# Kernel optimization log

Measured on AMD Instinct MI355X. Metric: run time of the kernel, lower is better.

## Reference

```python
import jax, jax.numpy as jnp
import numpy as np
from jax import lax

N_VOX = 100000   # occupied voxels
GRID = 160       # dense grid extent per axis
K = 5            # kernel size -> 125 offsets
K3 = K * K * K
IMG_C, PTS_C, OUT_C = 64, 32, 16
EPS = 1e-5


def _build_coords_and_kernel_map():
    """Random unique voxel coords + kernel map: nbr[n,k] = row index of voxel at
    coords[n]+offset[k], or N_VOX (sentinel -> zero feature) if unoccupied."""
    rng = np.random.default_rng(0)
    flat = rng.choice(GRID ** 3, size=N_VOX, replace=False)
    coords = np.stack(np.unravel_index(flat, (GRID, GRID, GRID)), axis=1).astype(np.int64)
    B = GRID + 4  # shift coords by +2 so offsets in [-2,2] never wrap
    enc = ((coords[:, 0] + 2) * B + (coords[:, 1] + 2)) * B + (coords[:, 2] + 2)
    order = np.argsort(enc)
    enc_s = enc[order]
    offs = np.stack(np.meshgrid(np.arange(-2, 3), np.arange(-2, 3), np.arange(-2, 3), indexing='ij'), axis=-1).reshape(-1, 3)
    nbr = np.full((N_VOX, K3), N_VOX, dtype=np.int32)
    for k, (dx, dy, dz) in enumerate(offs):
        qe = enc + ((dx * B + dy) * B + dz)
        pos = np.clip(np.searchsorted(enc_s, qe), 0, N_VOX - 1)
        hit = enc_s[pos] == qe
        nbr[:, k] = np.where(hit, order[pos].astype(np.int32), np.int32(N_VOX))
    return nbr


def setup_inputs() -> dict:
    nbr_idx = jnp.asarray(_build_coords_and_kernel_map())
    key = jax.random.key(0)
    ks = jax.random.split(key, 20)
    def w(k, shape, fan):
        return jax.random.normal(k, shape, jnp.float32) * (1.0 / np.sqrt(fan))
    def bn(k0, k1, k2, k3):
        g = jax.random.uniform(k0, (OUT_C,), jnp.float32) + 0.5
        b = jax.random.normal(k1, (OUT_C,), jnp.float32) * 0.1
        m = jax.random.normal(k2, (OUT_C,), jnp.float32) * 0.1
        v = jax.random.uniform(k3, (OUT_C,), jnp.float32) + 0.5
        return g, b, m, v
    bn_img = bn(ks[2], ks[3], ks[4], ks[5])
    bn_pts = bn(ks[7], ks[8], ks[9], ks[10])
    bn_vis = bn(ks[12], ks[13], ks[14], ks[15])
    return {
        'img_voxel_feats': jax.random.normal(ks[0], (N_VOX, IMG_C), jnp.float32),
        'pts_voxel_feats': jax.random.normal(ks[1], (N_VOX, PTS_C), jnp.float32),
        'nbr_idx': nbr_idx,
        'W_img': w(ks[16], (K3, IMG_C, OUT_C), K3 * IMG_C),
        'bn_img_g': bn_img[0], 'bn_img_b': bn_img[1], 'bn_img_m': bn_img[2], 'bn_img_v': bn_img[3],
        'W_pts': w(ks[17], (K3, PTS_C, OUT_C), K3 * PTS_C),
        'bn_pts_g': bn_pts[0], 'bn_pts_b': bn_pts[1], 'bn_pts_m': bn_pts[2], 'bn_pts_v': bn_pts[3],
        'W_vis1': w(ks[18], (K3, 2 * OUT_C, OUT_C), K3 * 2 * OUT_C),
        'bn_vis_g': bn_vis[0], 'bn_vis_b': bn_vis[1], 'bn_vis_m': bn_vis[2], 'bn_vis_v': bn_vis[3],
        'W_vis2': w(ks[19], (OUT_C, 1), OUT_C),
    }


def _sparse_conv(feats, W, nbr_idx):
    # gather-GEMM-scatter sparse conv; sentinel row N -> zero feature
    feats_pad = jnp.concatenate([feats, jnp.zeros((1, feats.shape[1]), feats.dtype)], axis=0)
    init = jnp.zeros((feats.shape[0], W.shape[2]), feats.dtype)
    def step(acc, wk_ik):
        W_k, idx_k = wk_ik  # [Cin,Cout], [N]
        return acc + feats_pad[idx_k] @ W_k, None
    out, _ = lax.scan(step, init, (W, nbr_idx.T))
    return out


def _bn_relu(x, g, b, m, v):
    return jax.nn.relu((x - m) * (g * lax.rsqrt(v + EPS)) + b)


def reference(img_voxel_feats, pts_voxel_feats, nbr_idx,
              W_img, bn_img_g, bn_img_b, bn_img_m, bn_img_v,
              W_pts, bn_pts_g, bn_pts_b, bn_pts_m, bn_pts_v,
              W_vis1, bn_vis_g, bn_vis_b, bn_vis_m, bn_vis_v,
              W_vis2):
    img = _bn_relu(_sparse_conv(img_voxel_feats, W_img, nbr_idx), bn_img_g, bn_img_b, bn_img_m, bn_img_v)
    pts = _bn_relu(_sparse_conv(pts_voxel_feats, W_pts, nbr_idx), bn_pts_g, bn_pts_b, bn_pts_m, bn_pts_v)
    cat = jnp.concatenate([img, pts], axis=1)  # [N, 2*OUT_C]
    h = _bn_relu(_sparse_conv(cat, W_vis1, nbr_idx), bn_vis_g, bn_vis_b, bn_vis_m, bn_vis_v)
    vis_w = jax.nn.sigmoid(h @ W_vis2)  # [N,1]
    return vis_w * img + (1.0 - vis_w) * pts
```

## Files before the change

kernel.cpp:

```cpp
#include <hip/hip_runtime.h>

#define N_VOX 100000
#define K3 125
#define CENTER_K 62
#define BVOX 128
#define NBLK 782
#define EPSF 1e-5f

#define WIT 0
#define WPT 128000
#define WVT 192000
#define LST 256000
#define CAT (256000 + NBLK * 1024)

#define DOT4(f_, g_) ((f_).x*(g_).x + (f_).y*(g_).y + (f_).z*(g_).z + (f_).w*(g_).w)

__global__ __launch_bounds__(256) void prep_transpose(
    const float* __restrict__ Wi, const float* __restrict__ Wp,
    const float* __restrict__ Wv, float* __restrict__ ws)
{
    int i = blockIdx.x * 256 + threadIdx.x;
    if (i < 125 * 64 * 16) {
        int k = i >> 10, r = i & 1023;
        int c = r >> 4, o = r & 15;
        int cs = c >> 4, t = (c >> 2) & 3, e = c & 3;
        ws[WIT + k * 1024 + t * 256 + (cs * 16 + o) * 4 + e] = Wi[i];
    }
    if (i < 125 * 32 * 16) {
        int k = i / 512, r = i % 512;
        int c = r >> 4, o = r & 15;
        int cs = c >> 3, t = (c >> 2) & 1, e = c & 3;
        ws[WPT + k * 512 + t * 256 + (cs * 16 + o) * 4 + e] = Wp[i];
        ws[WVT + k * 512 + t * 256 + (cs * 16 + o) * 4 + e] = Wv[i];
    }
}

__global__ __launch_bounds__(512, 6) void convA(
    const float* __restrict__ fimg, const float* __restrict__ fpts,
    const int* __restrict__ nbr, float* __restrict__ ws,
    const float* __restrict__ gi, const float* __restrict__ bi,
    const float* __restrict__ mi, const float* __restrict__ vi,
    const float* __restrict__ gp, const float* __restrict__ bp,
    const float* __restrict__ mp, const float* __restrict__ vp)
{
    __shared__ int s_kcnt[128];
    __shared__ int s_scan[128];
    __shared__ int s_koff[128];
    __shared__ int s_list[768];
    __shared__ float s_acc[BVOX][32];
    __shared__ int s_next;

    const int tid = threadIdx.x, lane = tid & 63, wv = tid >> 6;
    const int blk = blockIdx.x;
    const int gbase = blk * BVOX;
    const int vcount = min(BVOX, N_VOX - gbase);
    const int q = lane >> 4;

    if (tid < 128) s_kcnt[tid] = 0;
    if (tid == 0) s_next = 0;
    __syncthreads();

    const int TOTE = vcount * K3;
    const int* nrow = nbr + (size_t)gbase * K3;
    for (int e = tid; e < TOTE; e += 512) {
        int idx = nrow[e];
        int k = e % K3;
        if (idx < N_VOX && k != CENTER_K) atomicAdd(&s_kcnt[k], 1);
    }
    __syncthreads();

    if (tid < 128) s_scan[tid] = (tid < K3) ? s_kcnt[tid] : 0;
    __syncthreads();
    for (int d = 1; d < 128; d <<= 1) {
        int v = 0;
        if (tid < 128 && tid >= d) v = s_scan[tid - d];
        __syncthreads();
        if (tid < 128) s_scan[tid] += v;
        __syncthreads();
    }
    if (tid < 128) s_koff[tid] = (tid == 0) ? 0 : s_scan[tid - 1];
    __syncthreads();
    if (tid < 128) s_kcnt[tid] = s_koff[tid];
    __syncthreads();

    for (int e = tid; e < TOTE; e += 512) {
        int idx = nrow[e];
        int k = e % K3;
        if (idx < N_VOX && k != CENTER_K) {
            int ln = e / K3;
            int pos = atomicAdd(&s_kcnt[k], 1);
            s_list[pos] = (ln << 17) | idx;
        }
    }
    __syncthreads();

    {
        int tot = s_koff[K3];
        int* dst = (int*)(ws + LST) + (size_t)blk * 1024;
        if (tid < 126) dst[tid] = s_koff[tid];
        for (int p = tid; p < tot; p += 512) dst[128 + p] = s_list[p];
    }

    const float4* __restrict__ fi4 = (const float4*)fimg;
    const float4* __restrict__ fp4 = (const float4*)fpts;

    {
        float4 cwi[4], cwp[2];
        const float4* WI4 = (const float4*)(ws + WIT + CENTER_K * 1024);
        const float4* WP4 = (const float4*)(ws + WPT + CENTER_K * 512);
        #pragma unroll
        for (int t = 0; t < 4; ++t) cwi[t] = WI4[t * 64 + lane];
        #pragma unroll
        for (int t = 0; t < 2; ++t) cwp[t] = WP4[t * 64 + lane];
        for (int i = 0; i < 16; ++i) {
            int ln = wv * 16 + i;
            if (ln >= vcount) break;
            int n = gbase + ln;
            const float4* fr = fi4 + (size_t)n * 16 + q * 4;
            const float4* gr = fp4 + (size_t)n * 8 + q * 2;
            float aI = DOT4(fr[0], cwi[0]) + DOT4(fr[1], cwi[1])
                     + DOT4(fr[2], cwi[2]) + DOT4(fr[3], cwi[3]);
            float aP = DOT4(gr[0], cwp[0]) + DOT4(gr[1], cwp[1]);
            aI += __shfl_xor(aI, 16); aI += __shfl_xor(aI, 32);
            aP += __shfl_xor(aP, 16); aP += __shfl_xor(aP, 32);
            if (lane < 32) s_acc[ln][lane] = (lane < 16) ? aI : aP;
        }
    }
    __syncthreads();

    while (true) {
        int s;
        if (lane == 0) s = atomicAdd(&s_next, 1);
        s = __shfl(s, 0);
        if (s >= K3) break;
        int pbeg = s_koff[s], pend = s_koff[s + 1];
        if (pbeg == pend) continue;
        float4 swi[4], swp[2];
        const float4* WI4 = (const float4*)(ws + WIT + s * 1024);
        const float4* WP4 = (const float4*)(ws + WPT + s * 512);
        #pragma unroll
        for (int t = 0; t < 4; ++t) swi[t] = WI4[t * 64 + lane];
        #pragma unroll
        for (int t = 0; t < 2; ++t) swp[t] = WP4[t * 64 + lane];
        for (int p = pbeg; p < pend; ++p) {
            int ent = s_list[p];
            int ln = ent >> 17, j = ent & 0x1FFFF;
            const float4* fr = fi4 + (size_t)j * 16 + q * 4;
            const float4* gr = fp4 + (size_t)j * 8 + q * 2;
            float aI = DOT4(fr[0], swi[0]) + DOT4(fr[1], swi[1])
                     + DOT4(fr[2], swi[2]) + DOT4(fr[3], swi[3]);
            float aP = DOT4(gr[0], swp[0]) + DOT4(gr[1], swp[1]);
            aI += __shfl_xor(aI, 16); aI += __shfl_xor(aI, 32);
            aP += __shfl_xor(aP, 16); aP += __shfl_xor(aP, 32);
            if (lane < 32) atomicAdd(&s_acc[ln][lane], (lane < 16) ? aI : aP);
        }
    }
    __syncthreads();

    {
        int c = tid & 31;
        float g, b, m, v;
        if (c < 16) { g = gi[c]; b = bi[c]; m = mi[c]; v = vi[c]; }
        else        { g = gp[c - 16]; b = bp[c - 16]; m = mp[c - 16]; v = vp[c - 16]; }
        float sc = g * rsqrtf(v + EPSF);
        float* cat = ws + CAT;
        for (int r = 0; r < 8; ++r) {
            int ln = (tid >> 5) + r * 16;
            if (ln < vcount)
                cat[(size_t)(gbase + ln) * 32 + c] =
                    fmaxf((s_acc[ln][c] - m) * sc + b, 0.f);
        }
    }
}

__global__ __launch_bounds__(512, 6) void convB(
    float* __restrict__ ws,
    const float* __restrict__ gv, const float* __restrict__ bv,
    const float* __restrict__ mv, const float* __restrict__ vv,
    const float* __restrict__ w2, float* __restrict__ out)
{
    __shared__ int s_koff[128];
    __shared__ int s_list[768];
    __shared__ float s_acc[BVOX][16];
    __shared__ int s_next;

    const int tid = threadIdx.x, lane = tid & 63, wv = tid >> 6;
    const int blk = blockIdx.x;
    const int gbase = blk * BVOX;
    const int vcount = min(BVOX, N_VOX - gbase);
    const int q = lane >> 4, o = lane & 15;

    const int* src = (const int*)(ws + LST) + (size_t)blk * 1024;
    if (tid < 126) s_koff[tid] = src[tid];
    if (tid == 0) s_next = 0;
    __syncthreads();
    int tot = s_koff[K3];
    for (int p = tid; p < tot; p += 512) s_list[p] = src[128 + p];

    const float4* __restrict__ c4 = (const float4*)(ws + CAT);

    {
        float4 cwv[2];
        const float4* WV4 = (const float4*)(ws + WVT + CENTER_K * 512);
        #pragma unroll
        for (int t = 0; t < 2; ++t) cwv[t] = WV4[t * 64 + lane];
        for (int i = 0; i < 16; ++i) {
            int ln = wv * 16 + i;
            if (ln >= vcount) break;
            int n = gbase + ln;
            const float4* cr = c4 + (size_t)n * 8 + q * 2;
            float aV = DOT4(cr[0], cwv[0]) + DOT4(cr[1], cwv[1]);
            aV += __shfl_xor(aV, 16); aV += __shfl_xor(aV, 32);
            if (lane < 16) s_acc[ln][o] = aV;
        }
    }
    __syncthreads();

    while (true) {
        int s;
        if (lane == 0) s = atomicAdd(&s_next, 1);
        s = __shfl(s, 0);
        if (s >= K3) break;
        int pbeg = s_koff[s], pend = s_koff[s + 1];
        if (pbeg == pend) continue;
        float4 swv[2];
        const float4* WV4 = (const float4*)(ws + WVT + s * 512);
        #pragma unroll
        for (int t = 0; t < 2; ++t) swv[t] = WV4[t * 64 + lane];
        for (int p = pbeg; p < pend; ++p) {
            int ent = s_list[p];
            int ln = ent >> 17, j = ent & 0x1FFFF;
            const float4* cr = c4 + (size_t)j * 8 + q * 2;
            float aV = DOT4(cr[0], swv[0]) + DOT4(cr[1], swv[1]);
            aV += __shfl_xor(aV, 16); aV += __shfl_xor(aV, 32);
            if (lane < 16) atomicAdd(&s_acc[ln][o], aV);
        }
    }
    __syncthreads();

    {
        float sV = gv[o] * rsqrtf(vv[o] + EPSF);
        float bV = bv[o], mV = mv[o], w2_ = w2[o];
        const float* cat = ws + CAT;
        for (int r = 0; r < 4; ++r) {
            int ln = (tid >> 4) + r * 32;
            float h = 0.f, xi = 0.f, xp = 0.f;
            if (ln < vcount) {
                int n = gbase + ln;
                h = fmaxf((s_acc[ln][o] - mV) * sV + bV, 0.f);
                xi = cat[(size_t)n * 32 + o];
                xp = cat[(size_t)n * 32 + 16 + o];
            }
            float ph = h * w2_;
            ph += __shfl_xor(ph, 1); ph += __shfl_xor(ph, 2);
            ph += __shfl_xor(ph, 4); ph += __shfl_xor(ph, 8);
            if (ln < vcount) {
                float vis = 1.f / (1.f + expf(-ph));
                out[(size_t)(gbase + ln) * 16 + o] = vis * xi + (1.f - vis) * xp;
            }
        }
    }
}

extern "C" void kernel_launch(void* const* d_in, const int* in_sizes, int n_in,
                              void* d_out, int out_size, void* d_ws, size_t ws_size,
                              hipStream_t stream) {
    const float* fimg = (const float*)d_in[0];
    const float* fpts = (const float*)d_in[1];
    const int*   nbr  = (const int*)d_in[2];
    const float* Wimg = (const float*)d_in[3];
    const float* gi = (const float*)d_in[4];
    const float* bi = (const float*)d_in[5];
    const float* mi = (const float*)d_in[6];
    const float* vi = (const float*)d_in[7];
    const float* Wpts = (const float*)d_in[8];
    const float* gp = (const float*)d_in[9];
    const float* bp = (const float*)d_in[10];
    const float* mp = (const float*)d_in[11];
    const float* vp = (const float*)d_in[12];
    const float* Wvis = (const float*)d_in[13];
    const float* gv = (const float*)d_in[14];
    const float* bv = (const float*)d_in[15];
    const float* mv = (const float*)d_in[16];
    const float* vv = (const float*)d_in[17];
    const float* w2 = (const float*)d_in[18];
    float* out = (float*)d_out;
    float* ws = (float*)d_ws;

    hipLaunchKernelGGL(prep_transpose, dim3(500), dim3(256), 0, stream,
                       Wimg, Wpts, Wvis, ws);
    hipLaunchKernelGGL(convA, dim3(NBLK), dim3(512), 0, stream,
                       fimg, fpts, nbr, ws, gi, bi, mi, vi, gp, bp, mp, vp);
    hipLaunchKernelGGL(convB, dim3(NBLK), dim3(512), 0, stream,
                       ws, gv, bv, mv, vv, w2, out);
}
```

Measured before the change: 229.7 us.

## Build per-block neighbor lists in separate compacting kernel, halve block size

Moves the kernel-map scan out of convA into a separate global build kernel that compacts valid (k, local voxel, neighbor) entries per block with global atomics, so convA only reads the short compacted list instead of rescanning 125 entries per voxel twice. Also changes the weight layout so each half-wave handles one gather (two pairs processed per wave with 32 lanes each), and shrinks blocks to 256 threads. The list is capped at 640 entries per block, so any overflow would silently drop neighbors, and an extra memset plus kernel launch is added.

```diff
diff --git a/kernel.cpp b/kernel.cpp
--- a/kernel.cpp
+++ b/kernel.cpp
@@ -3,15 +3,19 @@
 #define N_VOX 100000
 #define K3 125
 #define CENTER_K 62
-#define BVOX 128
+#define TVOX 128
 #define NBLK 782
+#define CAP2 640
 #define EPSF 1e-5f
 
 #define WIT 0
 #define WPT 128000
 #define WVT 192000
-#define LST 256000
-#define CAT (256000 + NBLK * 1024)
+#define GCNT 256000
+#define GLIST 257024
+#define KOFF  757504
+#define SLIST 857600
+#define CAT   1358080
 
 #define DOT4(f_, g_) ((f_).x*(g_).x + (f_).y*(g_).y + (f_).z*(g_).z + (f_).w*(g_).w)
 
@@ -22,150 +26,177 @@
     int i = blockIdx.x * 256 + threadIdx.x;
     if (i < 125 * 64 * 16) {
         int k = i >> 10, r = i & 1023;
-        int c = r >> 4, o = r & 15;
-        int cs = c >> 4, t = (c >> 2) & 3, e = c & 3;
-        ws[WIT + k * 1024 + t * 256 + (cs * 16 + o) * 4 + e] = Wi[i];
+        int c = r >> 4, oo = r & 15;
+        int qq = c >> 5, t = (c >> 2) & 7, e = c & 3;
+        ws[WIT + k * 1024 + t * 128 + (qq * 16 + oo) * 4 + e] = Wi[i];
     }
     if (i < 125 * 32 * 16) {
-        int k = i / 512, r = i % 512;
-        int c = r >> 4, o = r & 15;
-        int cs = c >> 3, t = (c >> 2) & 1, e = c & 3;
-        ws[WPT + k * 512 + t * 256 + (cs * 16 + o) * 4 + e] = Wp[i];
-        ws[WVT + k * 512 + t * 256 + (cs * 16 + o) * 4 + e] = Wv[i];
-    }
-}
-
-__global__ __launch_bounds__(512, 6) void convA(
+        int k = i >> 9, r = i & 511;
+        int c = r >> 4, oo = r & 15;
+        int qq = c >> 4, t = (c >> 2) & 3, e = c & 3;
+        ws[WPT + k * 512 + t * 128 + (qq * 16 + oo) * 4 + e] = Wp[i];
+        ws[WVT + k * 512 + t * 128 + (qq * 16 + oo) * 4 + e] = Wv[i];
+    }
+}
+
+__global__ __launch_bounds__(256) void build(const int* __restrict__ nbr,
+                                             float* __restrict__ ws)
+{
+    int* gcnt = (int*)(ws + GCNT);
+    int* glist = (int*)(ws + GLIST);
+    const int TOT4 = (N_VOX * K3) / 4;
+    const int4* n4 = (const int4*)nbr;
+    for (int i4 = blockIdx.x * 256 + threadIdx.x; i4 < TOT4; i4 += gridDim.x * 256) {
+        int4 v = n4[i4];
+        int base = i4 * 4;
+        int idxs[4] = {v.x, v.y, v.z, v.w};
+        #pragma unroll
+        for (int j = 0; j < 4; ++j) {
+            int idx = idxs[j];
+            int i = base + j;
+            unsigned n = (unsigned)i / K3;
+            int k = i - (int)n * K3;
+            if (idx < N_VOX && k != CENTER_K) {
+                int blk = n >> 7, ln = n & 127;
+                int pos = atomicAdd(&gcnt[blk], 1);
+                if (pos < CAP2)
+                    glist[(size_t)blk * CAP2 + pos] = (k << 24) | (ln << 17) | idx;
+            }
+        }
+    }
+}
+
+__global__ __launch_bounds__(256, 3) void convA(
     const float* __restrict__ fimg, const float* __restrict__ fpts,
-    const int* __restrict__ nbr, float* __restrict__ ws,
+    float* __restrict__ ws,
     const float* __restrict__ gi, const float* __restrict__ bi,
     const float* __restrict__ mi, const float* __restrict__ vi,
     const float* __restrict__ gp, const float* __restrict__ bp,
     const float* __restrict__ mp, const float* __restrict__ vp)
 {
     __shared__ int s_kcnt[128];
-    __shared__ int s_scan[128];
     __shared__ int s_koff[128];
-    __shared__ int s_list[768];
-    __shared__ float s_acc[BVOX][32];
+    __shared__ int s_list[CAP2];
+    __shared__ float s_acc[TVOX][32];
     __shared__ int s_next;
 
-    const int tid = threadIdx.x, lane = tid & 63, wv = tid >> 6;
-    const int blk = blockIdx.x;
-    const int gbase = blk * BVOX;
-    const int vcount = min(BVOX, N_VOX - gbase);
-    const int q = lane >> 4;
+    const int tid = threadIdx.x;
+    const int lane = tid & 63, wv = tid >> 6;
+    const int l32 = lane & 31, qp = (lane >> 4) & 1, o = lane & 15, s2 = lane >> 5;
+    const int blk = blockIdx.x, gbase = blk * TVOX;
+    const int vcount = min(TVOX, N_VOX - gbase);
 
     if (tid < 128) s_kcnt[tid] = 0;
     if (tid == 0) s_next = 0;
     __syncthreads();
 
-    const int TOTE = vcount * K3;
-    const int* nrow = nbr + (size_t)gbase * K3;
-    for (int e = tid; e < TOTE; e += 512) {
-        int idx = nrow[e];
-        int k = e % K3;
-        if (idx < N_VOX && k != CENTER_K) atomicAdd(&s_kcnt[k], 1);
-    }
-    __syncthreads();
-
-    if (tid < 128) s_scan[tid] = (tid < K3) ? s_kcnt[tid] : 0;
+    const int cnt = min(((const int*)(ws + GCNT))[blk], CAP2);
+    const int* gl = (const int*)(ws + GLIST) + (size_t)blk * CAP2;
+
+    for (int p = tid; p < cnt; p += 256)
+        atomicAdd(&s_kcnt[((unsigned)gl[p]) >> 24], 1);
+    __syncthreads();
+
+    if (tid < 128) s_koff[tid] = (tid < K3) ? s_kcnt[tid] : 0;
     __syncthreads();
     for (int d = 1; d < 128; d <<= 1) {
         int v = 0;
-        if (tid < 128 && tid >= d) v = s_scan[tid - d];
+        if (tid < 128 && tid >= d) v = s_koff[tid - d];
         __syncthreads();
-        if (tid < 128) s_scan[tid] += v;
+        if (tid < 128) s_koff[tid] += v;
         __syncthreads();
     }
-    if (tid < 128) s_koff[tid] = (tid == 0) ? 0 : s_scan[tid - 1];
-    __syncthreads();
-    if (tid < 128) s_kcnt[tid] = s_koff[tid];
-    __syncthreads();
-
-    for (int e = tid; e < TOTE; e += 512) {
-        int idx = nrow[e];
-        int k = e % K3;
-        if (idx < N_VOX && k != CENTER_K) {
-            int ln = e / K3;
-            int pos = atomicAdd(&s_kcnt[k], 1);
-            s_list[pos] = (ln << 17) | idx;
-        }
-    }
-    __syncthreads();
-
-    {
-        int tot = s_koff[K3];
-        int* dst = (int*)(ws + LST) + (size_t)blk * 1024;
-        if (tid < 126) dst[tid] = s_koff[tid];
-        for (int p = tid; p < tot; p += 512) dst[128 + p] = s_list[p];
+    if (tid < 128) s_kcnt[tid] = tid ? s_koff[tid - 1] : 0;
+    __syncthreads();
+
+    for (int p = tid; p < cnt; p += 256) {
+        int ent = gl[p];
+        int pos = atomicAdd(&s_kcnt[((unsigned)ent) >> 24], 1);
+        s_list[pos] = ent;
+    }
+    __syncthreads();
+
+    {
+        int tot = s_koff[K3 - 1];
+        int* kfo = (int*)(ws + KOFF) + (size_t)blk * 128;
+        int* slo = (int*)(ws + SLIST) + (size_t)blk * CAP2;
+        if (tid < K3) kfo[tid] = s_koff[tid];
+        for (int p = tid; p < tot; p += 256) slo[p] = s_list[p];
     }
 
     const float4* __restrict__ fi4 = (const float4*)fimg;
     const float4* __restrict__ fp4 = (const float4*)fpts;
 
     {
-        float4 cwi[4], cwp[2];
-        const float4* WI4 = (const float4*)(ws + WIT + CENTER_K * 1024);
-        const float4* WP4 = (const float4*)(ws + WPT + CENTER_K * 512);
-        #pragma unroll
-        for (int t = 0; t < 4; ++t) cwi[t] = WI4[t * 64 + lane];
-        #pragma unroll
-        for (int t = 0; t < 2; ++t) cwp[t] = WP4[t * 64 + lane];
+        float4 wi[8], wp[4];
+        const float4* WI = (const float4*)(ws + WIT + CENTER_K * 1024);
+        const float4* WP = (const float4*)(ws + WPT + CENTER_K * 512);
+        #pragma unroll
+        for (int t = 0; t < 8; ++t) wi[t] = WI[t * 32 + l32];
+        #pragma unroll
+        for (int t = 0; t < 4; ++t) wp[t] = WP[t * 32 + l32];
         for (int i = 0; i < 16; ++i) {
-            int ln = wv * 16 + i;
-            if (ln >= vcount) break;
-            int n = gbase + ln;
-            const float4* fr = fi4 + (size_t)n * 16 + q * 4;
-            const float4* gr = fp4 + (size_t)n * 8 + q * 2;
-            float aI = DOT4(fr[0], cwi[0]) + DOT4(fr[1], cwi[1])
-                     + DOT4(fr[2], cwi[2]) + DOT4(fr[3], cwi[3]);
-            float aP = DOT4(gr[0], cwp[0]) + DOT4(gr[1], cwp[1]);
-            aI += __shfl_xor(aI, 16); aI += __shfl_xor(aI, 32);
-            aP += __shfl_xor(aP, 16); aP += __shfl_xor(aP, 32);
-            if (lane < 32) s_acc[ln][lane] = (lane < 16) ? aI : aP;
+            int ln = wv * 32 + i * 2 + s2;
+            bool val = ln < vcount;
+            int j = gbase + (val ? ln : 0);
+            const float4* F = fi4 + (size_t)j * 16 + qp * 8;
+            const float4* G = fp4 + (size_t)j * 8 + qp * 4;
+            float aI = 0.f, aP = 0.f;
+            #pragma unroll
+            for (int t = 0; t < 8; ++t) aI += DOT4(F[t], wi[t]);
+            #pragma unroll
+            for (int t = 0; t < 4; ++t) aP += DOT4(G[t], wp[t]);
+            aI += __shfl_xor(aI, 16);
+            aP += __shfl_xor(aP, 16);
+            if (val) s_acc[ln][qp * 16 + o] = qp ? aP : aI;
         }
     }
     __syncthreads();
 
     while (true) {
-        int s;
-        if (lane == 0) s = atomicAdd(&s_next, 1);
-        s = __shfl(s, 0);
-        if (s >= K3) break;
-        int pbeg = s_koff[s], pend = s_koff[s + 1];
-        if (pbeg == pend) continue;
-        float4 swi[4], swp[2];
-        const float4* WI4 = (const float4*)(ws + WIT + s * 1024);
-        const float4* WP4 = (const float4*)(ws + WPT + s * 512);
-        #pragma unroll
-        for (int t = 0; t < 4; ++t) swi[t] = WI4[t * 64 + lane];
-        #pragma unroll
-        for (int t = 0; t < 2; ++t) swp[t] = WP4[t * 64 + lane];
-        for (int p = pbeg; p < pend; ++p) {
-            int ent = s_list[p];
-            int ln = ent >> 17, j = ent & 0x1FFFF;
-            const float4* fr = fi4 + (size_t)j * 16 + q * 4;
-            const float4* gr = fp4 + (size_t)j * 8 + q * 2;
-            float aI = DOT4(fr[0], swi[0]) + DOT4(fr[1], swi[1])
-                     + DOT4(fr[2], swi[2]) + DOT4(fr[3], swi[3]);
-            float aP = DOT4(gr[0], swp[0]) + DOT4(gr[1], swp[1]);
-            aI += __shfl_xor(aI, 16); aI += __shfl_xor(aI, 32);
-            aP += __shfl_xor(aP, 16); aP += __shfl_xor(aP, 32);
-            if (lane < 32) atomicAdd(&s_acc[ln][lane], (lane < 16) ? aI : aP);
-        }
-    }
-    __syncthreads();
-
-    {
-        int c = tid & 31;
+        int sseg;
+        if (lane == 0) sseg = atomicAdd(&s_next, 1);
+        sseg = __shfl(sseg, 0);
+        if (sseg >= K3) break;
+        int pbeg = sseg ? s_koff[sseg - 1] : 0;
+        int pend = s_koff[sseg];
+        if (pbeg >= pend) continue;
+        float4 wi[8], wp[4];
+        const float4* WI = (const float4*)(ws + WIT + sseg * 1024);
+        const float4* WP = (const float4*)(ws + WPT + sseg * 512);
+        #pragma unroll
+        for (int t = 0; t < 8; ++t) wi[t] = WI[t * 32 + l32];
+        #pragma unroll
+        for (int t = 0; t < 4; ++t) wp[t] = WP[t * 32 + l32];
+        for (int p = pbeg; p < pend; p += 2) {
+            int pp = p + s2;
+            bool val = pp < pend;
+            int ent = s_list[val ? pp : p];
+            int ln = (ent >> 17) & 127, j = ent & 0x1FFFF;
+            const float4* F = fi4 + (size_t)j * 16 + qp * 8;
+            const float4* G = fp4 + (size_t)j * 8 + qp * 4;
+            float aI = 0.f, aP = 0.f;
+            #pragma unroll
+            for (int t = 0; t < 8; ++t) aI += DOT4(F[t], wi[t]);
+            #pragma unroll
+            for (int t = 0; t < 4; ++t) aP += DOT4(G[t], wp[t]);
+            aI += __shfl_xor(aI, 16);
+            aP += __shfl_xor(aP, 16);
+            if (val) atomicAdd(&s_acc[ln][qp * 16 + o], qp ? aP : aI);
+        }
+    }
+    __syncthreads();
+
+    {
+        const int c = tid & 31;
         float g, b, m, v;
         if (c < 16) { g = gi[c]; b = bi[c]; m = mi[c]; v = vi[c]; }
         else        { g = gp[c - 16]; b = bp[c - 16]; m = mp[c - 16]; v = vp[c - 16]; }
         float sc = g * rsqrtf(v + EPSF);
         float* cat = ws + CAT;
-        for (int r = 0; r < 8; ++r) {
-            int ln = (tid >> 5) + r * 16;
+        const int grp = tid >> 5;
+        for (int r = 0; r < 16; ++r) {
+            int ln = r * 8 + grp;
             if (ln < vcount)
                 cat[(size_t)(gbase + ln) * 32 + c] =
                     fmaxf((s_acc[ln][c] - m) * sc + b, 0.f);
@@ -173,67 +204,75 @@
     }
 }
 
-__global__ __launch_bounds__(512, 6) void convB(
+__global__ __launch_bounds__(256, 3) void convB(
     float* __restrict__ ws,
     const float* __restrict__ gv, const float* __restrict__ bv,
     const float* __restrict__ mv, const float* __restrict__ vv,
     const float* __restrict__ w2, float* __restrict__ out)
 {
     __shared__ int s_koff[128];
-    __shared__ int s_list[768];
-    __shared__ float s_acc[BVOX][16];
+    __shared__ int s_list[CAP2];
+    __shared__ float s_acc[TVOX][16];
     __shared__ int s_next;
 
-    const int tid = threadIdx.x, lane = tid & 63, wv = tid >> 6;
-    const int blk = blockIdx.x;
-    const int gbase = blk * BVOX;
-    const int vcount = min(BVOX, N_VOX - gbase);
-    const int q = lane >> 4, o = lane & 15;
-
-    const int* src = (const int*)(ws + LST) + (size_t)blk * 1024;
-    if (tid < 126) s_koff[tid] = src[tid];
+    const int tid = threadIdx.x;
+    const int lane = tid & 63, wv = tid >> 6;
+    const int l32 = lane & 31, qp = (lane >> 4) & 1, o = lane & 15, s2 = lane >> 5;
+    const int blk = blockIdx.x, gbase = blk * TVOX;
+    const int vcount = min(TVOX, N_VOX - gbase);
+
     if (tid == 0) s_next = 0;
-    __syncthreads();
-    int tot = s_koff[K3];
-    for (int p = tid; p < tot; p += 512) s_list[p] = src[128 + p];
+    const int* kfo = (const int*)(ws + KOFF) + (size_t)blk * 128;
+    if (tid < K3) s_koff[tid] = kfo[tid];
+    __syncthreads();
+    const int tot = s_koff[K3 - 1];
+    const int* slo = (const int*)(ws + SLIST) + (size_t)blk * CAP2;
+    for (int p = tid; p < tot; p += 256) s_list[p] = slo[p];
 
     const float4* __restrict__ c4 = (const float4*)(ws + CAT);
 
     {
-        float4 cwv[2];
-        const float4* WV4 = (const float4*)(ws + WVT + CENTER_K * 512);
-        #pragma unroll
-        for (int t = 0; t < 2; ++t) cwv[t] = WV4[t * 64 + lane];
+        float4 wvr[4];
+        const float4* WV = (const float4*)(ws + WVT + CENTER_K * 512);
+        #pragma unroll
+        for (int t = 0; t < 4; ++t) wvr[t] = WV[t * 32 + l32];
         for (int i = 0; i < 16; ++i) {
-            int ln = wv * 16 + i;
-            if (ln >= vcount) break;
-            int n = gbase + ln;
-            const float4* cr = c4 + (size_t)n * 8 + q * 2;
-            float aV = DOT4(cr[0], cwv[0]) + DOT4(cr[1], cwv[1]);
-            aV += __shfl_xor(aV, 16); aV += __shfl_xor(aV, 32);
-            if (lane < 16) s_acc[ln][o] = aV;
+            int ln = wv * 32 + i * 2 + s2;
+            bool val = ln < vcount;
+            int j = gbase + (val ? ln : 0);
+            const float4* F = c4 + (size_t)j * 8 + qp * 4;
+            float aV = 0.f;
+            #pragma unroll
+            for (int t = 0; t < 4; ++t) aV += DOT4(F[t], wvr[t]);
+            aV += __shfl_xor(aV, 16);
+            if (val && qp == 0) s_acc[ln][o] = aV;
         }
     }
     __syncthreads();
 
     while (true) {
-        int s;
-        if (lane == 0) s = atomicAdd(&s_next, 1);
-        s = __shfl(s, 0);
-        if (s >= K3) break;
-        int pbeg = s_koff[s], pend = s_koff[s + 1];
-        if (pbeg == pend) continue;
-        float4 swv[2];
-        const float4* WV4 = (const float4*)(ws + WVT + s * 512);
-        #pragma unroll
-        for (int t = 0; t < 2; ++t) swv[t] = WV4[t * 64 + lane];
-        for (int p = pbeg; p < pend; ++p) {
-            int ent = s_list[p];
-            int ln = ent >> 17, j = ent & 0x1FFFF;
-            const float4* cr = c4 + (size_t)j * 8 + q * 2;
-            float aV = DOT4(cr[0], swv[0]) + DOT4(cr[1], swv[1]);
-            aV += __shfl_xor(aV, 16); aV += __shfl_xor(aV, 32);
-            if (lane < 16) atomicAdd(&s_acc[ln][o], aV);
+        int sseg;
+        if (lane == 0) sseg = atomicAdd(&s_next, 1);
+        sseg = __shfl(sseg, 0);
+        if (sseg >= K3) break;
+        int pbeg = sseg ? s_koff[sseg - 1] : 0;
+        int pend = s_koff[sseg];
+        if (pbeg >= pend) continue;
+        float4 wvr[4];
+        const float4* WV = (const float4*)(ws + WVT + sseg * 512);
+        #pragma unroll
+        for (int t = 0; t < 4; ++t) wvr[t] = WV[t * 32 + l32];
+        for (int p = pbeg; p < pend; p += 2) {
+            int pp = p + s2;
+            bool val = pp < pend;
+            int ent = s_list[val ? pp : p];
+            int ln = (ent >> 17) & 127, j = ent & 0x1FFFF;
+            const float4* F = c4 + (size_t)j * 8 + qp * 4;
+            float aV = 0.f;
+            #pragma unroll
+            for (int t = 0; t < 4; ++t) aV += DOT4(F[t], wvr[t]);
+            aV += __shfl_xor(aV, 16);
+            if (val && qp == 0) atomicAdd(&s_acc[ln][o], aV);
         }
     }
     __syncthreads();
@@ -242,8 +281,9 @@
         float sV = gv[o] * rsqrtf(vv[o] + EPSF);
         float bV = bv[o], mV = mv[o], w2_ = w2[o];
         const float* cat = ws + CAT;
-        for (int r = 0; r < 4; ++r) {
-            int ln = (tid >> 4) + r * 32;
+        const int grp = tid >> 4;
+        for (int r = 0; r < 8; ++r) {
+            int ln = r * 16 + grp;
             float h = 0.f, xi = 0.f, xp = 0.f;
             if (ln < vcount) {
                 int n = gbase + ln;
@@ -287,10 +327,12 @@
     float* out = (float*)d_out;
     float* ws = (float*)d_ws;
 
+    hipMemsetAsync(ws + GCNT, 0, 1024 * sizeof(int), stream);
     hipLaunchKernelGGL(prep_transpose, dim3(500), dim3(256), 0, stream,
                        Wimg, Wpts, Wvis, ws);
-    hipLaunchKernelGGL(convA, dim3(NBLK), dim3(512), 0, stream,
-                       fimg, fpts, nbr, ws, gi, bi, mi, vi, gp, bp, mp, vp);
-    hipLaunchKernelGGL(convB, dim3(NBLK), dim3(512), 0, stream,
+    hipLaunchKernelGGL(build, dim3(4096), dim3(256), 0, stream, nbr, ws);
+    hipLaunchKernelGGL(convA, dim3(NBLK), dim3(256), 0, stream,
+                       fimg, fpts, ws, gi, bi, mi, vi, gp, bp, mp, vp);
+    hipLaunchKernelGGL(convB, dim3(NBLK), dim3(256), 0, stream,
                        ws, gv, bv, mv, vv, w2, out);
 }
```

After: 602.3 us. 2.62x slower.
